# Performance work log

Hardware: AMD Instinct MI355X
Metric: run time of the kernel (lower is better)

Reference implementation:

```python
import jax, jax.numpy as jnp
import numpy as np

# Episode constants (match init_kwargs / input shapes)
B, WAY, SHOT, K = 2, 5, 5, 5
Q_NUM, DIM, HW = 30, 64, 441
BN_EPS = 1e-5


def _episode(q, s, gamma, beta, w3):
    """q: [Q, D, HW] query features; s: [WAY*SHOT, D, HW] support features."""
    # --- cosine logits between mean-pooled query and class prototypes ---
    q_pool = q.mean(axis=2)                                        # [Q, D]
    proto = s.mean(axis=2).reshape(WAY, SHOT, DIM).mean(axis=1)    # [WAY, D]
    qF = q_pool / jnp.linalg.norm(q_pool, axis=-1, keepdims=True)
    pF = proto / jnp.linalg.norm(proto, axis=-1, keepdims=True)
    logits_cos = qF @ pF.T                                         # [Q, WAY]

    # --- spatially L2-normalized descriptors (norm over HW axis, as in torch) ---
    q_norm = q / jnp.linalg.norm(q, axis=2, keepdims=True)         # [Q, D, HW]
    s_norm = s / jnp.linalg.norm(s, axis=2, keepdims=True)         # [WAY*SHOT, D, HW]
    s_l = s_norm.reshape(WAY, SHOT * DIM, HW)                      # [WAY, S*D, HW]
    s_p = jnp.transpose(s_norm, (0, 2, 1)).reshape(WAY, SHOT * HW, DIM)  # [WAY, S*HW, D]

    # channel-level similarity: [Q, WAY, D, SHOT*D], top-k over last axis
    ip_l = jnp.einsum('qdh,wkh->qwdk', q_norm, s_l)
    top_l, _ = jax.lax.top_k(ip_l, K)
    sim_l = top_l.sum(axis=(2, 3))                                 # [Q, WAY]

    # pixel-level similarity: [Q, WAY, HW, SHOT*HW], top-k over last axis
    ip_p = jnp.einsum('qhd,wkd->qwhk', jnp.transpose(q_norm, (0, 2, 1)), s_p)
    top_p, _ = jax.lax.top_k(ip_p, K)
    sim_p = top_p.sum(axis=(2, 3))                                 # [Q, WAY]

    # --- BatchNorm1d(3*WAY), training mode (per-episode batch stats) ---
    feats = jnp.concatenate([logits_cos, sim_l, sim_p], axis=1)    # [Q, 3*WAY]
    mu = feats.mean(axis=0)
    var = feats.var(axis=0)  # biased, as torch BN uses for normalization
    feats_bn = (feats - mu) / jnp.sqrt(var + BN_EPS) * gamma + beta

    # --- Conv1d(1,1,kernel=3,dilation=5,no bias): out length 3*WAY-10 ---
    L = 3 * WAY
    out = w3[0] * feats_bn[:, :L - 10] + w3[1] * feats_bn[:, 5:L - 5] + w3[2] * feats_bn[:, 10:]
    return out                                                      # [Q, WAY]


def setup_inputs() -> dict:
    key = jax.random.key(0)
    k1, k2, k3 = jax.random.split(key, 3)
    return {
        'input1_batch': jax.random.normal(k1, (B * Q_NUM, DIM, HW), dtype=jnp.float32),
        'input2_batch': jax.random.normal(k2, (B * WAY * SHOT, DIM, HW), dtype=jnp.float32),
        'gamma': jnp.ones((3 * WAY,), dtype=jnp.float32),
        'beta': jnp.zeros((3 * WAY,), dtype=jnp.float32),
        'conv_w': jax.random.normal(k3, (1, 1, 3), dtype=jnp.float32),
    }


def reference(input1_batch, input2_batch, gamma, beta, conv_w):
    q = input1_batch.reshape(B, Q_NUM, DIM, HW)
    s = input2_batch.reshape(B, WAY * SHOT, DIM, HW)
    w3 = conv_w.reshape(3)
    sim = jax.vmap(lambda qi, si: _episode(qi, si, gamma, beta, w3))(q, s)
    return sim  # [B, Q_NUM, WAY]
```

## Files before the change

### kernel.cpp

```cpp
#include <hip/hip_runtime.h>
#include <math.h>


typedef __attribute__((ext_vector_type(8))) short bf16x8;
typedef __attribute__((ext_vector_type(4))) float f32x4;

#define MFMA16(a, b, c) __builtin_amdgcn_mfma_f32_16x16x32_bf16((a), (b), (c), 0, 0, 0)

__device__ __forceinline__ unsigned short to_bf16(float v) {
    unsigned int u = __float_as_uint(v);
    unsigned int r = u + 0x7FFFu + ((u >> 16) & 1u);
    return (unsigned short)(r >> 16);
}

__device__ __forceinline__ void ins5(float m[5], float v) {
    m[4] = __builtin_amdgcn_fmed3f(v, m[4], m[3]);
    m[3] = __builtin_amdgcn_fmed3f(v, m[3], m[2]);
    m[2] = __builtin_amdgcn_fmed3f(v, m[2], m[1]);
    m[1] = __builtin_amdgcn_fmed3f(v, m[1], m[0]);
    m[0] = fmaxf(m[0], v);
}

__global__ __launch_bounds__(256) void k1_rownorm(const float* __restrict__ in1,
                                                  const float* __restrict__ in2,
                                                  float* __restrict__ inv_norm,
                                                  float* __restrict__ pool) {
    int wv = threadIdx.x >> 6;
    int lane = threadIdx.x & 63;
    int rid = blockIdx.x * 4 + wv;
    const float* src = (rid < 3840) ? (in1 + (size_t)rid * 441)
                                    : (in2 + (size_t)(rid - 3840) * 441);
    float s = 0.f, ss = 0.f;
#pragma unroll
    for (int i = 0; i < 7; ++i) {
        int h = lane + i * 64;
        if (h < 441) { float v = src[h]; s += v; ss = fmaf(v, v, ss); }
    }
#pragma unroll
    for (int off = 32; off > 0; off >>= 1) {
        s += __shfl_xor(s, off, 64);
        ss += __shfl_xor(ss, off, 64);
    }
    if (lane == 0) {
        inv_norm[rid] = 1.0f / sqrtf(ss);
        pool[rid] = s * (1.0f / 441.0f);
    }
}

__global__ __launch_bounds__(256, 4) void pack_all(const float* __restrict__ in1,
                                                   const float* __restrict__ in2,
                                                   const float* __restrict__ inv_norm,
                                                   const float* __restrict__ pool,
                                                   uint4* __restrict__ Pq,
                                                   uint4* __restrict__ Ps,
                                                   uint4* __restrict__ Al,
                                                   uint4* __restrict__ Bl,
                                                   float* __restrict__ feats) {
    int bid = blockIdx.x;
    int tid = threadIdx.x;
    unsigned short hs[8];
    if (bid < 840) {
        int idx = bid * 256 + tid;
        int lane = idx & 63;
        int ks = (idx >> 6) & 1;
        int rest = idx >> 7;
        int gcs = rest % 840, e = rest / 840;
        int q = gcs / 28, cs = gcs % 28;
        int h = cs * 16 + (lane & 15);
        int d0 = ks * 32 + ((lane >> 4) << 3);
        int rowq = (e * 30 + q) * 64;
#pragma unroll
        for (int j = 0; j < 8; ++j) {
            int d = d0 + j;
            float v = (h < 441) ? in1[(size_t)(rowq + d) * 441 + h] * inv_norm[rowq + d] : 0.f;
            hs[j] = to_bf16(v);
        }
        uint4 H;
        H.x = hs[0] | (hs[1] << 16); H.y = hs[2] | (hs[3] << 16);
        H.z = hs[4] | (hs[5] << 16); H.w = hs[6] | (hs[7] << 16);
        Pq[idx] = H;
    } else if (bid < 1530) {
        int idx = (bid - 840) * 256 + tid;
        int lane = idx & 63;
        int ks = (idx >> 6) & 1;
        int rest = idx >> 7;
        int kt = rest % 138, ew = rest / 138;
        int kidx = kt * 16 + (lane & 15);
        bool valid = kidx < 2205;
        int kc = valid ? kidx : 0;
        int sh = kc / 441;
        int h = kc - sh * 441;
        int e = ew / 5, w = ew % 5;
        int srow = ((e * 25 + w * 5 + sh) * 64);
        int d0 = ks * 32 + ((lane >> 4) << 3);
#pragma unroll
        for (int j = 0; j < 8; ++j) {
            int d = d0 + j;
            float v = valid ? in2[(size_t)(srow + d) * 441 + h] * inv_norm[3840 + srow + d] : 0.f;
            hs[j] = to_bf16(v);
        }
        uint4 H;
        H.x = hs[0] | (hs[1] << 16); H.y = hs[2] | (hs[3] << 16);
        H.z = hs[4] | (hs[5] << 16); H.w = hs[6] | (hs[7] << 16);
        Ps[idx] = H;
    } else if (bid < 2230) {
        int idx = (bid - 1530) * 256 + tid;
        int lane = idx & 63;
        int t2 = idx >> 6;
        int ks = t2 % 14;
        int t3 = t2 / 14;
        int rt = t3 % 20, ew = t3 / 20;
        int e = ew / 5, w = ew % 5;
        int row = rt * 16 + (lane & 15);
        int sh = row >> 6, dp = row & 63;
        int srow = (e * 25 + w * 5 + sh) * 64 + dp;
        int h0 = ks * 32 + ((lane >> 4) << 3);
        const float* src = in2 + (size_t)srow * 441;
        float inv = inv_norm[3840 + srow];
#pragma unroll
        for (int j = 0; j < 8; ++j) {
            int h = h0 + j;
            float v = (h < 441) ? src[h] * inv : 0.f;
            hs[j] = to_bf16(v);
        }
        uint4 H;
        H.x = hs[0] | (hs[1] << 16); H.y = hs[2] | (hs[3] << 16);
        H.z = hs[4] | (hs[5] << 16); H.w = hs[6] | (hs[7] << 16);
        Al[idx] = H;
    } else if (bid < 3070) {
        int idx = (bid - 2230) * 256 + tid;
        int lane = idx & 63;
        int t2 = idx >> 6;
        int ks = t2 % 14;
        int t3 = t2 / 14;
        int gct = t3 % 120, e = t3 / 120;
        int col = gct * 16 + (lane & 15);
        int q = col >> 6, d = col & 63;
        int qrow = (e * 30 + q) * 64 + d;
        int h0 = ks * 32 + ((lane >> 4) << 3);
        const float* src = in1 + (size_t)qrow * 441;
        float inv = inv_norm[qrow];
#pragma unroll
        for (int j = 0; j < 8; ++j) {
            int h = h0 + j;
            float v = (h < 441) ? src[h] * inv : 0.f;
            hs[j] = to_bf16(v);
        }
        uint4 H;
        H.x = hs[0] | (hs[1] << 16); H.y = hs[2] | (hs[3] << 16);
        H.z = hs[4] | (hs[5] << 16); H.w = hs[6] | (hs[7] << 16);
        Bl[idx] = H;
    } else {
        int e = bid - 3070;
        __shared__ float qp[30 * 64], pr[5 * 64], qn[30], pn[5];
        int t = tid;
        for (int li = t; li < 1920; li += 256) qp[li] = pool[e * 30 * 64 + li];
        for (int li = t; li < 320; li += 256) {
            int w = li >> 6, d = li & 63;
            float sm = 0.f;
            for (int sh = 0; sh < 5; ++sh) sm += pool[(60 + e * 25 + w * 5 + sh) * 64 + d];
            pr[li] = sm * 0.2f;
        }
        __syncthreads();
        if (t < 30) {
            float ss = 0.f;
            for (int d = 0; d < 64; ++d) { float v = qp[t * 64 + d]; ss = fmaf(v, v, ss); }
            qn[t] = 1.0f / sqrtf(ss);
        }
        if (t >= 32 && t < 37) {
            int w = t - 32; float ss = 0.f;
            for (int d = 0; d < 64; ++d) { float v = pr[w * 64 + d]; ss = fmaf(v, v, ss); }
            pn[w] = 1.0f / sqrtf(ss);
        }
        __syncthreads();
        if (t < 150) {
            int q = t / 5, w = t % 5;
            float dp = 0.f;
            for (int d = 0; d < 64; ++d) dp = fmaf(qp[q * 64 + d], pr[w * 64 + d], dp);
            feats[(e * 30 + q) * 15 + w] = dp * qn[q] * pn[w];
        }
    }
}

template <int NRR>
__device__ __forceinline__ void chan_pass(int rr0, int ew, int e, int q, int wv, int lane,
                                          const bf16x8* __restrict__ Bl,
                                          const bf16x8* __restrict__ Al,
                                          float m[4][5]) {
    f32x4 cc[NRR][4];
#pragma unroll
    for (int r = 0; r < NRR; ++r)
#pragma unroll
        for (int s = 0; s < 4; ++s) cc[r][s] = (f32x4){0.f, 0.f, 0.f, 0.f};
    for (int ks = 0; ks < 14; ++ks) {
        bf16x8 bh[4];
#pragma unroll
        for (int s = 0; s < 4; ++s)
            bh[s] = Bl[((e * 120 + q * 4 + s) * 14 + ks) * 64 + lane];
#pragma unroll
        for (int r = 0; r < NRR; ++r) {
            bf16x8 ah = Al[((ew * 20 + wv * 5 + rr0 + r) * 14 + ks) * 64 + lane];
#pragma unroll
            for (int s = 0; s < 4; ++s) cc[r][s] = MFMA16(ah, bh[s], cc[r][s]);
        }
    }
#pragma unroll
    for (int r = 0; r < NRR; ++r)
#pragma unroll
        for (int s = 0; s < 4; ++s)
#pragma unroll
            for (int g = 0; g < 4; ++g) ins5(m[s], cc[r][s][g]);
}

__global__ __launch_bounds__(256, 2) void k56(const bf16x8* __restrict__ Pq,
                                              const bf16x8* __restrict__ Ps,
                                              const bf16x8* __restrict__ Bl,
                                              const bf16x8* __restrict__ Al,
                                              float* __restrict__ part_p,
                                              float* __restrict__ siml) {
    __shared__ float SH[1280];
    int bid = blockIdx.x;
    int tid = threadIdx.x;
    int xcd = bid & 7;
    int slot = bid >> 3;
    int wv = tid >> 6, lane = tid & 63;
    const f32x4 ZV = {0.f, 0.f, 0.f, 0.f};

    if (slot < 263) {
        int p = xcd * 263 + slot;
        if (p >= 2100) return;
        int ew = p / 210;
        int gwave = p - ew * 210;
        int e = ew / 5, w = ew - (ew / 5) * 5;
        int q = gwave / 7;
        int ct0 = gwave * 4;
        int k0 = wv * 35;
        int kend = (wv == 3) ? 138 : k0 + 35;

        bf16x8 Bh[4][2];
#pragma unroll
        for (int s = 0; s < 4; ++s)
#pragma unroll
            for (int ks = 0; ks < 2; ++ks)
                Bh[s][ks] = Pq[((e * 840 + ct0 + s) * 2 + ks) * 64 + lane];

        float m[4][5];
#pragma unroll
        for (int s = 0; s < 4; ++s)
#pragma unroll
            for (int i = 0; i < 5; ++i) m[s][i] = -1e30f;

        int rowbase = (lane >> 4) * 4;
        const bf16x8* As = Ps + (size_t)(ew * 138) * 128 + lane;

        bf16x8 a0 = As[(size_t)k0 * 128];
        bf16x8 a1 = As[(size_t)k0 * 128 + 64];
        for (int kt = k0; kt < kend; ++kt) {
            int ktn = (kt + 1 < kend) ? kt + 1 : kt;
            bf16x8 n0 = As[(size_t)ktn * 128];
            bf16x8 n1 = As[(size_t)ktn * 128 + 64];
#pragma unroll
            for (int s = 0; s < 4; ++s) {
                f32x4 cv = MFMA16(a0, Bh[s][0], ZV);
                cv = MFMA16(a1, Bh[s][1], cv);
                if (kt == 137) {
#pragma unroll
                    for (int gg = 0; gg < 4; ++gg) {
                        float v = (rowbase + gg < 13) ? cv[gg] : -1e30f;
                        ins5(m[s], v);
                    }
                } else {
#pragma unroll
                    for (int gg = 0; gg < 4; ++gg) ins5(m[s], cv[gg]);
                }
            }
            a0 = n0; a1 = n1;
        }

#pragma unroll
        for (int mask = 16; mask <= 32; mask <<= 1) {
            float ov[4][5];
#pragma unroll
            for (int s = 0; s < 4; ++s)
#pragma unroll
                for (int i = 0; i < 5; ++i) ov[s][i] = __shfl_xor(m[s][i], mask, 64);
#pragma unroll
            for (int s = 0; s < 4; ++s)
#pragma unroll
                for (int i = 0; i < 5; ++i) ins5(m[s], ov[s][i]);
        }

        float (*Msh)[4][16][5] = (float (*)[4][16][5])SH;
        if (lane < 16) {
#pragma unroll
            for (int s = 0; s < 4; ++s)
#pragma unroll
                for (int i = 0; i < 5; ++i) Msh[wv][s][lane][i] = m[s][i];
        }
        __syncthreads();
        if (wv == 0) {
            int s = lane >> 4, col = lane & 15;
            float lst[5];
#pragma unroll
            for (int i = 0; i < 5; ++i) lst[i] = Msh[0][s][col][i];
#pragma unroll
            for (int w2 = 1; w2 < 4; ++w2)
#pragma unroll
                for (int i = 0; i < 5; ++i) ins5(lst, Msh[w2][s][col][i]);
            float s5 = lst[0] + lst[1] + lst[2] + lst[3] + lst[4];
            int h = ((ct0 + s) % 28) * 16 + col;
            s5 = (h < 441) ? s5 : 0.f;
#pragma unroll
            for (int mask = 1; mask <= 32; mask <<= 1) s5 += __shfl_xor(s5, mask, 64);
            if (lane == 0) {
                int sl = gwave - q * 7;
                part_p[((e * 30 + q) * 5 + w) * 7 + sl] = s5;
            }
        }
    } else {
        float (*Mred)[64][5] = (float (*)[64][5])SH;
        int c = xcd * 38 + (slot - 263);
        if (c >= 300) return;
        int ew = c / 30, q = c - ew * 30;
        int e = ew / 5, w = ew - (ew / 5) * 5;

        float m[4][5];
#pragma unroll
        for (int s = 0; s < 4; ++s)
#pragma unroll
            for (int i = 0; i < 5; ++i) m[s][i] = -1e30f;

        chan_pass<3>(0, ew, e, q, wv, lane, Bl, Al, m);
        chan_pass<2>(3, ew, e, q, wv, lane, Bl, Al, m);

#pragma unroll
        for (int mask = 16; mask <= 32; mask <<= 1) {
            float ov[4][5];
#pragma unroll
            for (int s = 0; s < 4; ++s)
#pragma unroll
                for (int i = 0; i < 5; ++i) ov[s][i] = __shfl_xor(m[s][i], mask, 64);
#pragma unroll
            for (int s = 0; s < 4; ++s)
#pragma unroll
                for (int i = 0; i < 5; ++i) ins5(m[s], ov[s][i]);
        }

        if (lane < 16) {
#pragma unroll
            for (int s = 0; s < 4; ++s)
#pragma unroll
                for (int i = 0; i < 5; ++i) Mred[wv][s * 16 + lane][i] = m[s][i];
        }
        __syncthreads();

        if (tid < 64) {
            float lst[5];
#pragma unroll
            for (int i = 0; i < 5; ++i) lst[i] = Mred[0][tid][i];
#pragma unroll
            for (int v2 = 1; v2 < 4; ++v2)
#pragma unroll
                for (int i = 0; i < 5; ++i) ins5(lst, Mred[v2][tid][i]);
            float s5 = lst[0] + lst[1] + lst[2] + lst[3] + lst[4];
#pragma unroll
            for (int mask = 1; mask <= 32; mask <<= 1) s5 += __shfl_xor(s5, mask, 64);
            if (tid == 0) siml[(e * 30 + q) * 5 + w] = s5;
        }
    }
}

__global__ __launch_bounds__(256) void k7_final(const float* __restrict__ feats,
                                                const float* __restrict__ siml,
                                                const float* __restrict__ part_p,
                                                const float* __restrict__ gamma,
                                                const float* __restrict__ beta,
                                                const float* __restrict__ convw,
                                                float* __restrict__ out) {
    int e = blockIdx.x;
    __shared__ float f[30 * 15], mu[15], inv[15];
    int t = threadIdx.x;
    if (t < 150) {
        int q = t / 5, w = t % 5;
        int pb = ((e * 30 + q) * 5 + w) * 7;
        float sp = 0.f;
#pragma unroll
        for (int s = 0; s < 7; ++s) sp += part_p[pb + s];
        f[q * 15 + w] = feats[(e * 30 + q) * 15 + w];
        f[q * 15 + 5 + w] = siml[(e * 30 + q) * 5 + w];
        f[q * 15 + 10 + w] = sp;
    }
    __syncthreads();
    if (t < 15) {
        float s1 = 0.f;
        for (int q = 0; q < 30; ++q) s1 += f[q * 15 + t];
        float mn = s1 * (1.0f / 30.0f);
        float s2 = 0.f;
        for (int q = 0; q < 30; ++q) { float d = f[q * 15 + t] - mn; s2 = fmaf(d, d, s2); }
        mu[t] = mn;
        inv[t] = 1.0f / sqrtf(s2 * (1.0f / 30.0f) + 1e-5f);
    }
    __syncthreads();
    if (t < 150) {
        int q = t / 5, j = t % 5;
        float w0 = convw[0], w1 = convw[1], w2 = convw[2];
        float b0 = (f[q * 15 + j]      - mu[j])      * inv[j]      * gamma[j]      + beta[j];
        float b1 = (f[q * 15 + 5 + j]  - mu[5 + j])  * inv[5 + j]  * gamma[5 + j]  + beta[5 + j];
        float b2 = (f[q * 15 + 10 + j] - mu[10 + j]) * inv[10 + j] * gamma[10 + j] + beta[10 + j];
        out[e * 150 + q * 5 + j] = w0 * b0 + w1 * b1 + w2 * b2;
    }
}

extern "C" void kernel_launch(void* const* d_in, const int* in_sizes, int n_in,
                              void* d_out, int out_size, void* d_ws, size_t ws_size,
                              hipStream_t stream) {
    const float* in1 = (const float*)d_in[0];
    const float* in2 = (const float*)d_in[1];
    const float* gamma = (const float*)d_in[2];
    const float* beta = (const float*)d_in[3];
    const float* convw = (const float*)d_in[4];
    float* out = (float*)d_out;

    char* ws = (char*)d_ws;
    float* inv_norm = (float*)(ws + 0);
    float* pool     = (float*)(ws + 28160);
    float* feats    = (float*)(ws + 56320);
    float* siml     = (float*)(ws + 59920);
    float* part_p   = (float*)(ws + 61120);
    size_t o = 69520;
    uint4* Pq = (uint4*)(ws + o); o += 3440640;
    uint4* Ps = (uint4*)(ws + o); o += 2826240;
    uint4* Al = (uint4*)(ws + o); o += 2867200;
    uint4* Bl = (uint4*)(ws + o); o += 3440640;

    k1_rownorm<<<dim3(1760), dim3(256), 0, stream>>>(in1, in2, inv_norm, pool);
    pack_all<<<dim3(3072), dim3(256), 0, stream>>>(in1, in2, inv_norm, pool,
                                                   Pq, Ps, Al, Bl, feats);
    k56<<<dim3(2408), dim3(256), 0, stream>>>((const bf16x8*)Pq, (const bf16x8*)Ps,
                                              (const bf16x8*)Bl, (const bf16x8*)Al,
                                              part_p, siml);
    k7_final<<<dim3(2), dim3(256), 0, stream>>>(feats, siml, part_p, gamma, beta, convw, out);
}
```

Baseline: 131.0 us.

## Split fused pixel/channel kernel and triple-buffer the pixel loop loads

The combined k56 kernel, which dispatched pixel-level and channel-level top-k work by block slot, is split into two kernels, k6_pix and k5_chan, launched back to back. The pixel kernel's K loop is unrolled by three and keeps three register tiles of prefetched support data in flight, so MFMA and top-5 insertion work overlaps more memory latency. The per-wave K range moves from 35 to 36 tiles so the unroll divides evenly. Running the two parts as separate launches removes the branch divergence and lets each kernel use its own register footprint. The cost is an extra launch, and the channel blocks can no longer fill gaps left by the pixel blocks.

```diff
diff --git a/kernel.cpp b/kernel.cpp
--- a/kernel.cpp
+++ b/kernel.cpp
@@ -182,42 +182,37 @@
     }
 }
 
-template <int NRR>
-__device__ __forceinline__ void chan_pass(int rr0, int ew, int e, int q, int wv, int lane,
-                                          const bf16x8* __restrict__ Bl,
-                                          const bf16x8* __restrict__ Al,
-                                          float m[4][5]) {
-    f32x4 cc[NRR][4];
-#pragma unroll
-    for (int r = 0; r < NRR; ++r)
-#pragma unroll
-        for (int s = 0; s < 4; ++s) cc[r][s] = (f32x4){0.f, 0.f, 0.f, 0.f};
-    for (int ks = 0; ks < 14; ++ks) {
-        bf16x8 bh[4];
-#pragma unroll
-        for (int s = 0; s < 4; ++s)
-            bh[s] = Bl[((e * 120 + q * 4 + s) * 14 + ks) * 64 + lane];
-#pragma unroll
-        for (int r = 0; r < NRR; ++r) {
-            bf16x8 ah = Al[((ew * 20 + wv * 5 + rr0 + r) * 14 + ks) * 64 + lane];
-#pragma unroll
-            for (int s = 0; s < 4; ++s) cc[r][s] = MFMA16(ah, bh[s], cc[r][s]);
-        }
-    }
-#pragma unroll
-    for (int r = 0; r < NRR; ++r)
-#pragma unroll
-        for (int s = 0; s < 4; ++s)
-#pragma unroll
-            for (int g = 0; g < 4; ++g) ins5(m[s], cc[r][s][g]);
-}
-
-__global__ __launch_bounds__(256, 2) void k56(const bf16x8* __restrict__ Pq,
-                                              const bf16x8* __restrict__ Ps,
-                                              const bf16x8* __restrict__ Bl,
-                                              const bf16x8* __restrict__ Al,
-                                              float* __restrict__ part_p,
-                                              float* __restrict__ siml) {
+#define PIXBODY(X0, X1, KIDX)                                              \
+    do {                                                                   \
+        _Pragma("unroll")                                                  \
+        for (int s = 0; s < 4; ++s) {                                      \
+            f32x4 cv = MFMA16(X0, Bh[s][0], ZV);                           \
+            cv = MFMA16(X1, Bh[s][1], cv);                                 \
+            _Pragma("unroll")                                              \
+            for (int gg = 0; gg < 4; ++gg) ins5(m[s], cv[gg]);             \
+        }                                                                  \
+        X0 = As[(size_t)((KIDX) + 3) * 128];                               \
+        X1 = As[(size_t)((KIDX) + 3) * 128 + 64];                          \
+    } while (0)
+
+#define PIXTAIL(X0, X1, KIDX)                                              \
+    do {                                                                   \
+        bool lastk = ((KIDX) == 137);                                      \
+        _Pragma("unroll")                                                  \
+        for (int s = 0; s < 4; ++s) {                                      \
+            f32x4 cv = MFMA16(X0, Bh[s][0], ZV);                           \
+            cv = MFMA16(X1, Bh[s][1], cv);                                 \
+            _Pragma("unroll")                                              \
+            for (int gg = 0; gg < 4; ++gg) {                               \
+                float v = (lastk && (rowbase + gg >= 13)) ? -1e30f : cv[gg]; \
+                ins5(m[s], v);                                             \
+            }                                                              \
+        }                                                                  \
+    } while (0)
+
+__global__ __launch_bounds__(256, 2) void k6_pix(const bf16x8* __restrict__ Pq,
+                                                 const bf16x8* __restrict__ Ps,
+                                                 float* __restrict__ part_p) {
     __shared__ float SH[1280];
     int bid = blockIdx.x;
     int tid = threadIdx.x;
@@ -226,147 +221,177 @@
     int wv = tid >> 6, lane = tid & 63;
     const f32x4 ZV = {0.f, 0.f, 0.f, 0.f};
 
-    if (slot < 263) {
-        int p = xcd * 263 + slot;
-        if (p >= 2100) return;
-        int ew = p / 210;
-        int gwave = p - ew * 210;
-        int e = ew / 5, w = ew - (ew / 5) * 5;
-        int q = gwave / 7;
-        int ct0 = gwave * 4;
-        int k0 = wv * 35;
-        int kend = (wv == 3) ? 138 : k0 + 35;
-
-        bf16x8 Bh[4][2];
-#pragma unroll
-        for (int s = 0; s < 4; ++s)
-#pragma unroll
-            for (int ks = 0; ks < 2; ++ks)
-                Bh[s][ks] = Pq[((e * 840 + ct0 + s) * 2 + ks) * 64 + lane];
-
-        float m[4][5];
-#pragma unroll
-        for (int s = 0; s < 4; ++s)
-#pragma unroll
-            for (int i = 0; i < 5; ++i) m[s][i] = -1e30f;
-
-        int rowbase = (lane >> 4) * 4;
-        const bf16x8* As = Ps + (size_t)(ew * 138) * 128 + lane;
-
-        bf16x8 a0 = As[(size_t)k0 * 128];
-        bf16x8 a1 = As[(size_t)k0 * 128 + 64];
-        for (int kt = k0; kt < kend; ++kt) {
-            int ktn = (kt + 1 < kend) ? kt + 1 : kt;
-            bf16x8 n0 = As[(size_t)ktn * 128];
-            bf16x8 n1 = As[(size_t)ktn * 128 + 64];
-#pragma unroll
-            for (int s = 0; s < 4; ++s) {
-                f32x4 cv = MFMA16(a0, Bh[s][0], ZV);
-                cv = MFMA16(a1, Bh[s][1], cv);
-                if (kt == 137) {
-#pragma unroll
-                    for (int gg = 0; gg < 4; ++gg) {
-                        float v = (rowbase + gg < 13) ? cv[gg] : -1e30f;
-                        ins5(m[s], v);
-                    }
-                } else {
-#pragma unroll
-                    for (int gg = 0; gg < 4; ++gg) ins5(m[s], cv[gg]);
-                }
-            }
-            a0 = n0; a1 = n1;
-        }
-
-#pragma unroll
-        for (int mask = 16; mask <= 32; mask <<= 1) {
-            float ov[4][5];
-#pragma unroll
-            for (int s = 0; s < 4; ++s)
-#pragma unroll
-                for (int i = 0; i < 5; ++i) ov[s][i] = __shfl_xor(m[s][i], mask, 64);
-#pragma unroll
-            for (int s = 0; s < 4; ++s)
-#pragma unroll
-                for (int i = 0; i < 5; ++i) ins5(m[s], ov[s][i]);
-        }
-
-        float (*Msh)[4][16][5] = (float (*)[4][16][5])SH;
-        if (lane < 16) {
-#pragma unroll
-            for (int s = 0; s < 4; ++s)
-#pragma unroll
-                for (int i = 0; i < 5; ++i) Msh[wv][s][lane][i] = m[s][i];
-        }
-        __syncthreads();
-        if (wv == 0) {
-            int s = lane >> 4, col = lane & 15;
-            float lst[5];
-#pragma unroll
-            for (int i = 0; i < 5; ++i) lst[i] = Msh[0][s][col][i];
-#pragma unroll
-            for (int w2 = 1; w2 < 4; ++w2)
-#pragma unroll
-                for (int i = 0; i < 5; ++i) ins5(lst, Msh[w2][s][col][i]);
-            float s5 = lst[0] + lst[1] + lst[2] + lst[3] + lst[4];
-            int h = ((ct0 + s) % 28) * 16 + col;
-            s5 = (h < 441) ? s5 : 0.f;
-#pragma unroll
-            for (int mask = 1; mask <= 32; mask <<= 1) s5 += __shfl_xor(s5, mask, 64);
-            if (lane == 0) {
-                int sl = gwave - q * 7;
-                part_p[((e * 30 + q) * 5 + w) * 7 + sl] = s5;
-            }
-        }
-    } else {
-        float (*Mred)[64][5] = (float (*)[64][5])SH;
-        int c = xcd * 38 + (slot - 263);
-        if (c >= 300) return;
-        int ew = c / 30, q = c - ew * 30;
-        int e = ew / 5, w = ew - (ew / 5) * 5;
-
-        float m[4][5];
-#pragma unroll
-        for (int s = 0; s < 4; ++s)
-#pragma unroll
-            for (int i = 0; i < 5; ++i) m[s][i] = -1e30f;
-
-        chan_pass<3>(0, ew, e, q, wv, lane, Bl, Al, m);
-        chan_pass<2>(3, ew, e, q, wv, lane, Bl, Al, m);
-
-#pragma unroll
-        for (int mask = 16; mask <= 32; mask <<= 1) {
-            float ov[4][5];
-#pragma unroll
-            for (int s = 0; s < 4; ++s)
-#pragma unroll
-                for (int i = 0; i < 5; ++i) ov[s][i] = __shfl_xor(m[s][i], mask, 64);
-#pragma unroll
-            for (int s = 0; s < 4; ++s)
-#pragma unroll
-                for (int i = 0; i < 5; ++i) ins5(m[s], ov[s][i]);
-        }
-
-        if (lane < 16) {
-#pragma unroll
-            for (int s = 0; s < 4; ++s)
-#pragma unroll
-                for (int i = 0; i < 5; ++i) Mred[wv][s * 16 + lane][i] = m[s][i];
-        }
-        __syncthreads();
-
-        if (tid < 64) {
-            float lst[5];
-#pragma unroll
-            for (int i = 0; i < 5; ++i) lst[i] = Mred[0][tid][i];
-#pragma unroll
-            for (int v2 = 1; v2 < 4; ++v2)
-#pragma unroll
-                for (int i = 0; i < 5; ++i) ins5(lst, Mred[v2][tid][i]);
-            float s5 = lst[0] + lst[1] + lst[2] + lst[3] + lst[4];
-#pragma unroll
-            for (int mask = 1; mask <= 32; mask <<= 1) s5 += __shfl_xor(s5, mask, 64);
-            if (tid == 0) siml[(e * 30 + q) * 5 + w] = s5;
-        }
+    int p = xcd * 263 + slot;
+    if (p >= 2100) return;
+    int ew = p / 210;
+    int gwave = p - ew * 210;
+    int e = ew / 5, w = ew - (ew / 5) * 5;
+    int q = gwave / 7;
+    int ct0 = gwave * 4;
+    int k0 = wv * 36;
+    int kend = (wv == 3) ? 138 : k0 + 36;
+    int T = (kend - k0 - 3) / 3;
+
+    bf16x8 Bh[4][2];
+#pragma unroll
+    for (int s = 0; s < 4; ++s)
+#pragma unroll
+        for (int ks = 0; ks < 2; ++ks)
+            Bh[s][ks] = Pq[((e * 840 + ct0 + s) * 2 + ks) * 64 + lane];
+
+    float m[4][5];
+#pragma unroll
+    for (int s = 0; s < 4; ++s)
+#pragma unroll
+        for (int i = 0; i < 5; ++i) m[s][i] = -1e30f;
+
+    int rowbase = (lane >> 4) * 4;
+    const bf16x8* As = Ps + (size_t)(ew * 138) * 128 + lane;
+
+    bf16x8 a0 = As[(size_t)(k0 + 0) * 128], a1 = As[(size_t)(k0 + 0) * 128 + 64];
+    bf16x8 b0 = As[(size_t)(k0 + 1) * 128], b1 = As[(size_t)(k0 + 1) * 128 + 64];
+    bf16x8 c0 = As[(size_t)(k0 + 2) * 128], c1 = As[(size_t)(k0 + 2) * 128 + 64];
+
+    int kt = k0;
+    for (int i = 0; i < T; ++i) {
+        PIXBODY(a0, a1, kt);
+        PIXBODY(b0, b1, kt + 1);
+        PIXBODY(c0, c1, kt + 2);
+        kt += 3;
+    }
+    PIXTAIL(a0, a1, kt);
+    PIXTAIL(b0, b1, kt + 1);
+    PIXTAIL(c0, c1, kt + 2);
+
+#pragma unroll
+    for (int mask = 16; mask <= 32; mask <<= 1) {
+        float ov[4][5];
+#pragma unroll
+        for (int s = 0; s < 4; ++s)
+#pragma unroll
+            for (int i = 0; i < 5; ++i) ov[s][i] = __shfl_xor(m[s][i], mask, 64);
+#pragma unroll
+        for (int s = 0; s < 4; ++s)
+#pragma unroll
+            for (int i = 0; i < 5; ++i) ins5(m[s], ov[s][i]);
+    }
+
+    float (*Msh)[4][16][5] = (float (*)[4][16][5])SH;
+    if (lane < 16) {
+#pragma unroll
+        for (int s = 0; s < 4; ++s)
+#pragma unroll
+            for (int i = 0; i < 5; ++i) Msh[wv][s][lane][i] = m[s][i];
+    }
+    __syncthreads();
+    if (wv == 0) {
+        int s = lane >> 4, col = lane & 15;
+        float lst[5];
+#pragma unroll
+        for (int i = 0; i < 5; ++i) lst[i] = Msh[0][s][col][i];
+#pragma unroll
+        for (int w2 = 1; w2 < 4; ++w2)
+#pragma unroll
+            for (int i = 0; i < 5; ++i) ins5(lst, Msh[w2][s][col][i]);
+        float s5 = lst[0] + lst[1] + lst[2] + lst[3] + lst[4];
+        int h = ((ct0 + s) % 28) * 16 + col;
+        s5 = (h < 441) ? s5 : 0.f;
+#pragma unroll
+        for (int mask = 1; mask <= 32; mask <<= 1) s5 += __shfl_xor(s5, mask, 64);
+        if (lane == 0) {
+            int sl = gwave - q * 7;
+            part_p[((e * 30 + q) * 5 + w) * 7 + sl] = s5;
+        }
+    }
+}
+
+template <int NRR>
+__device__ __forceinline__ void chan_pass(int rr0, int ew, int e, int q, int wv, int lane,
+                                          const bf16x8* __restrict__ Bl,
+                                          const bf16x8* __restrict__ Al,
+                                          float m[4][5]) {
+    f32x4 cc[NRR][4];
+#pragma unroll
+    for (int r = 0; r < NRR; ++r)
+#pragma unroll
+        for (int s = 0; s < 4; ++s) cc[r][s] = (f32x4){0.f, 0.f, 0.f, 0.f};
+    for (int ks = 0; ks < 14; ++ks) {
+        bf16x8 bh[4];
+#pragma unroll
+        for (int s = 0; s < 4; ++s)
+            bh[s] = Bl[((e * 120 + q * 4 + s) * 14 + ks) * 64 + lane];
+#pragma unroll
+        for (int r = 0; r < NRR; ++r) {
+            bf16x8 ah = Al[((ew * 20 + wv * 5 + rr0 + r) * 14 + ks) * 64 + lane];
+#pragma unroll
+            for (int s = 0; s < 4; ++s) cc[r][s] = MFMA16(ah, bh[s], cc[r][s]);
+        }
+    }
+#pragma unroll
+    for (int r = 0; r < NRR; ++r)
+#pragma unroll
+        for (int s = 0; s < 4; ++s)
+#pragma unroll
+            for (int g = 0; g < 4; ++g) ins5(m[s], cc[r][s][g]);
+}
+
+__global__ __launch_bounds__(256, 2) void k5_chan(const bf16x8* __restrict__ Bl,
+                                                  const bf16x8* __restrict__ Al,
+                                                  float* __restrict__ siml) {
+    __shared__ float Mred[4][64][5];
+    int bid = blockIdx.x;
+    int tid = threadIdx.x;
+    int xcd = bid & 7;
+    int slot = bid >> 3;
+    int wv = tid >> 6, lane = tid & 63;
+
+    int c = xcd * 38 + slot;
+    if (c >= 300) return;
+    int ew = c / 30, q = c - ew * 30;
+    int e = ew / 5, w = ew - (ew / 5) * 5;
+
+    float m[4][5];
+#pragma unroll
+    for (int s = 0; s < 4; ++s)
+#pragma unroll
+        for (int i = 0; i < 5; ++i) m[s][i] = -1e30f;
+
+    chan_pass<3>(0, ew, e, q, wv, lane, Bl, Al, m);
+    chan_pass<2>(3, ew, e, q, wv, lane, Bl, Al, m);
+
+#pragma unroll
+    for (int mask = 16; mask <= 32; mask <<= 1) {
+        float ov[4][5];
+#pragma unroll
+        for (int s = 0; s < 4; ++s)
+#pragma unroll
+            for (int i = 0; i < 5; ++i) ov[s][i] = __shfl_xor(m[s][i], mask, 64);
+#pragma unroll
+        for (int s = 0; s < 4; ++s)
+#pragma unroll
+            for (int i = 0; i < 5; ++i) ins5(m[s], ov[s][i]);
+    }
+
+    if (lane < 16) {
+#pragma unroll
+        for (int s = 0; s < 4; ++s)
+#pragma unroll
+            for (int i = 0; i < 5; ++i) Mred[wv][s * 16 + lane][i] = m[s][i];
+    }
+    __syncthreads();
+
+    if (tid < 64) {
+        float lst[5];
+#pragma unroll
+        for (int i = 0; i < 5; ++i) lst[i] = Mred[0][tid][i];
+#pragma unroll
+        for (int v2 = 1; v2 < 4; ++v2)
+#pragma unroll
+            for (int i = 0; i < 5; ++i) ins5(lst, Mred[v2][tid][i]);
+        float s5 = lst[0] + lst[1] + lst[2] + lst[3] + lst[4];
+#pragma unroll
+        for (int mask = 1; mask <= 32; mask <<= 1) s5 += __shfl_xor(s5, mask, 64);
+        if (tid == 0) siml[(e * 30 + q) * 5 + w] = s5;
     }
 }
 
@@ -436,8 +461,9 @@
     k1_rownorm<<<dim3(1760), dim3(256), 0, stream>>>(in1, in2, inv_norm, pool);
     pack_all<<<dim3(3072), dim3(256), 0, stream>>>(in1, in2, inv_norm, pool,
                                                    Pq, Ps, Al, Bl, feats);
-    k56<<<dim3(2408), dim3(256), 0, stream>>>((const bf16x8*)Pq, (const bf16x8*)Ps,
-                                              (const bf16x8*)Bl, (const bf16x8*)Al,
-                                              part_p, siml);
+    k6_pix<<<dim3(2104), dim3(256), 0, stream>>>((const bf16x8*)Pq, (const bf16x8*)Ps,
+                                                 part_p);
+    k5_chan<<<dim3(304), dim3(256), 0, stream>>>((const bf16x8*)Bl, (const bf16x8*)Al,
+                                                 siml);
     k7_final<<<dim3(2), dim3(256), 0, stream>>>(feats, siml, part_p, gamma, beta, convw, out);
 }
```

Result: faster. 127.3 us (-2.8%).
